# Performance work log

Hardware: AMD Instinct MI355X
Metric: run time of the kernel (lower is better)

Reference implementation:

```python
import jax, jax.numpy as jnp
import numpy as np

B, S, D = 8, 2048, 128

def setup_inputs() -> dict:
    key = jax.random.key(0)
    kq, kk, kv, km = jax.random.split(key, 4)
    q = jax.random.normal(kq, (B, S, D), dtype=jnp.float32)
    k = jax.random.normal(kk, (B, S, D), dtype=jnp.float32)
    v = jax.random.normal(kv, (B, S, D), dtype=jnp.float32)
    mask = jax.random.randint(km, (B, S), 0, 2).astype(bool)  # True = masked out
    return {"q": q, "k": k, "v": v, "mask": mask}

def reference(q, k, v, mask):
    scaler = np.sqrt(D).astype(np.float32)
    # score[b, i, j] = <q_i, k_j> / sqrt(d_k)
    score = jnp.einsum('bik,bjk->bij', q, k) / scaler
    score = score - jnp.max(score, axis=-1, keepdims=True)
    e = jnp.exp(score)
    # mask is (B, S_kv): broadcast across query positions, zero out masked keys
    e = jnp.where(mask[:, None, :], 0.0, e)
    a = e / jnp.sum(e, axis=-1, keepdims=True)
    c = jnp.einsum('bij,bjd->bid', a, v)
    return c
```

## Files before the change

kernel.cpp:

```cpp
#include <hip/hip_runtime.h>
#include <math.h>

typedef __attribute__((ext_vector_type(8))) short short8;
typedef __attribute__((ext_vector_type(4))) float floatx4;

namespace {
constexpr int Bn = 8;
constexpr int Sn = 2048;
constexpr int Dn = 128;
constexpr int BQ = 64;
constexpr int BK = 64;
constexpr int QTILES = Sn / BQ;
constexpr int NKB = Sn / BK;
constexpr int ROWS = Bn * Sn;
constexpr int NSPLIT = 4;
constexpr float SC2 = 0.12753102063642597f;
constexpr int TILE_USH = BK * Dn;
}

#if __has_builtin(__builtin_amdgcn_exp2f)
#define EXP2(x) __builtin_amdgcn_exp2f(x)
#else
#define EXP2(x) exp2f(x)
#endif

__device__ __forceinline__ unsigned short f2bf(float x) {
  union { float f; unsigned u; } a; a.f = x;
  unsigned r = a.u + 0x7fffu + ((a.u >> 16) & 1u);
  return (unsigned short)(r >> 16);
}

__device__ __forceinline__ void gl_lds16(const void* g, void* l, int lane) {
#if __has_builtin(__builtin_amdgcn_global_load_lds)
  (void)lane;
  __builtin_amdgcn_global_load_lds((const __attribute__((address_space(1))) unsigned int*)g,
                                   (__attribute__((address_space(3))) unsigned int*)l, 16, 0, 0);
#else
  *(float4*)((char*)l + lane * 16) = *(const float4*)g;
#endif
}

__global__ __launch_bounds__(256)
void prep(const float* __restrict__ kg, const float* __restrict__ vg,
          const unsigned char* __restrict__ mraw,
          unsigned short* __restrict__ Kpg, unsigned short* __restrict__ Vpg,
          float* __restrict__ mb2g) {
  __shared__ __align__(16) float Vf[64 * 136];
  const int p = blockIdx.x;
  const int b = p >> 5, kb = p & 31;
  const int t = threadIdx.x;

  unsigned wv = ((const unsigned int*)mraw)[t];
  int any1  = __syncthreads_or((wv & 0x0000ff00u) ? 1 : 0);
  int any23 = __syncthreads_or((wv & 0xffff0000u) ? 1 : 0);
  const int mlayout = any1 ? 1 : (any23 ? 2 : 0);
  if (kb == 0) {
    #pragma unroll
    for (int i = 0; i < 8; ++i) {
      int idx = i * 256 + t;
      int jj = b * Sn + idx;
      bool ms;
      if (mlayout == 1)      ms = mraw[jj] != 0;
      else if (mlayout == 2) ms = ((const float*)mraw)[jj] != 0.0f;
      else                   ms = ((const int*)mraw)[jj] != 0;
      mb2g[jj] = ms ? -1e30f : 0.0f;
    }
  }

  const int j  = t >> 2;
  const int og = t & 3;
  const size_t rowbase = ((size_t)(b * Sn + kb * 64 + j)) * 32 + og * 8;
  const float4* k4 = (const float4*)kg;
  const float4* v4 = (const float4*)vg;

  float4 kf[8];
  #pragma unroll
  for (int q = 0; q < 8; ++q) kf[q] = k4[rowbase + q];
  unsigned short* Krow = Kpg + (size_t)p * TILE_USH + j * 128;
  #pragma unroll
  for (int oo = 0; oo < 4; ++oo) {
    const int o = og * 4 + oo;
    short8 pk;
    float4 a = kf[oo * 2], bq = kf[oo * 2 + 1];
    pk[0] = (short)f2bf(a.x);  pk[1] = (short)f2bf(a.y);
    pk[2] = (short)f2bf(a.z);  pk[3] = (short)f2bf(a.w);
    pk[4] = (short)f2bf(bq.x); pk[5] = (short)f2bf(bq.y);
    pk[6] = (short)f2bf(bq.z); pk[7] = (short)f2bf(bq.w);
    *(short8*)(Krow + ((o ^ (j & 7)) * 8)) = pk;
  }

  #pragma unroll
  for (int q = 0; q < 8; ++q) {
    float4 f = v4[rowbase + q];
    *(float4*)&Vf[j * 136 + og * 32 + q * 4] = f;
  }
  __syncthreads();

  const int d = t >> 1, h = t & 1;
  unsigned short* Vrow = Vpg + (size_t)p * TILE_USH + d * 64;
  #pragma unroll
  for (int oo = 0; oo < 4; ++oo) {
    const int o = h * 4 + oo;
    short8 pk;
    #pragma unroll
    for (int i = 0; i < 8; ++i)
      pk[i] = (short)f2bf(Vf[(o * 8 + i) * 136 + d]);
    *(short8*)(Vrow + ((o ^ (d & 7)) * 8)) = pk;
  }
}

template<int SPLIT, bool DIRECT>
__global__ __launch_bounds__(256, 4)
void attn_fwd(const float* __restrict__ qg,
              const unsigned short* __restrict__ Kpg,
              const unsigned short* __restrict__ Vpg,
              const float* __restrict__ mb2g,
              float* __restrict__ outg, float* __restrict__ Op,
              float* __restrict__ Mp, float* __restrict__ Lp) {
  __shared__ __align__(16) unsigned short Khi[TILE_USH];
  __shared__ __align__(16) unsigned short Vt[TILE_USH];
  __shared__ __align__(16) unsigned short Pq[4 * 16 * 64];

  const int tid = threadIdx.x;
  const int bid = blockIdx.x;
  const int b   = bid & 7;
  const int q0  = ((bid >> 3) & (QTILES - 1)) * BQ;
  const int s   = bid >> 8;
  const int kb0 = s * (NKB / SPLIT);
  const int kbN = kb0 + NKB / SPLIT;
  const int w   = tid >> 6;
  const int L   = tid & 63;
  const int g   = L >> 4;
  const int c   = L & 15;
  const int sw  = c & 7;

  short8 qh[4], ql[4];
  {
    const float* qrow = qg + (size_t)(b * Sn + q0 + w * 16 + c) * Dn + g * 8;
    #pragma unroll
    for (int kk = 0; kk < 4; ++kk) {
      #pragma unroll
      for (int j = 0; j < 8; ++j) {
        float x = qrow[kk * 32 + j];
        unsigned short hi = f2bf(x);
        union { unsigned u; float f; } hv; hv.u = ((unsigned)hi) << 16;
        qh[kk][j] = (short)hi;
        ql[kk][j] = (short)f2bf(x - hv.f);
      }
    }
  }

  float m_i = -INFINITY, l_i = 0.0f;
  floatx4 O[8];
  #pragma unroll
  for (int n2 = 0; n2 < 8; ++n2) O[n2] = (floatx4){0.f, 0.f, 0.f, 0.f};

  unsigned short* pwave = Pq + w * 1024;
  const int stagebase = w * 4096;

  for (int kb = kb0; kb < kbN; ++kb) {
    __syncthreads();

    {
      const char* kt = (const char*)(Kpg + (size_t)(b * NKB + kb) * TILE_USH);
      const char* vt = (const char*)(Vpg + (size_t)(b * NKB + kb) * TILE_USH);
      #pragma unroll
      for (int i = 0; i < 4; ++i) {
        const int off = stagebase + i * 1024;
        gl_lds16(kt + off + L * 16, (char*)Khi + off, L);
        gl_lds16(vt + off + L * 16, (char*)Vt + off, L);
      }
    }
    __syncthreads();

    const float4* mb4 = (const float4*)(mb2g + b * Sn + kb * BK);
    float4 mbv[4];
    #pragma unroll
    for (int nt = 0; nt < 4; ++nt) mbv[nt] = mb4[nt * 4 + g];

    floatx4 acc[4];
    #pragma unroll
    for (int nt = 0; nt < 4; ++nt) acc[nt] = (floatx4){0.f, 0.f, 0.f, 0.f};
    #pragma unroll
    for (int kk = 0; kk < 4; ++kk) {
      const int ko = ((kk * 4 + g) ^ sw) * 8;
      #pragma unroll
      for (int nt = 0; nt < 4; ++nt) {
        short8 kf = *(const short8*)&Khi[(nt * 16 + c) * 128 + ko];
        acc[nt] = __builtin_amdgcn_mfma_f32_16x16x32_bf16(kf, qh[kk], acc[nt], 0, 0, 0);
        acc[nt] = __builtin_amdgcn_mfma_f32_16x16x32_bf16(kf, ql[kk], acc[nt], 0, 0, 0);
      }
    }

    #pragma unroll
    for (int nt = 0; nt < 4; ++nt) {
      acc[nt][0] = fmaf(acc[nt][0], SC2, mbv[nt].x);
      acc[nt][1] = fmaf(acc[nt][1], SC2, mbv[nt].y);
      acc[nt][2] = fmaf(acc[nt][2], SC2, mbv[nt].z);
      acc[nt][3] = fmaf(acc[nt][3], SC2, mbv[nt].w);
    }
    float mx = -INFINITY;
    #pragma unroll
    for (int nt = 0; nt < 4; ++nt)
      #pragma unroll
      for (int r = 0; r < 4; ++r) mx = fmaxf(mx, acc[nt][r]);
    mx = fmaxf(mx, __shfl_xor(mx, 16));
    mx = fmaxf(mx, __shfl_xor(mx, 32));
    const float mnew = fmaxf(m_i, mx);
    const float alpha = EXP2(m_i - mnew);
    float rs = 0.0f;
    #pragma unroll
    for (int nt = 0; nt < 4; ++nt)
      #pragma unroll
      for (int r = 0; r < 4; ++r) {
        float e = EXP2(acc[nt][r] - mnew);
        acc[nt][r] = e;
        rs += e;
      }
    rs += __shfl_xor(rs, 16);
    rs += __shfl_xor(rs, 32);
    l_i = l_i * alpha + rs;
    m_i = mnew;

    #pragma unroll
    for (int nt = 0; nt < 4; ++nt) {
      ushort4 pk = make_ushort4(f2bf(acc[nt][0]), f2bf(acc[nt][1]),
                                f2bf(acc[nt][2]), f2bf(acc[nt][3]));
      const int oct = nt * 2 + (g >> 1);
      *(ushort4*)&pwave[c * 64 + ((oct ^ sw) * 8) + (g & 1) * 4] = pk;
    }

    #pragma unroll
    for (int n2 = 0; n2 < 8; ++n2)
      #pragma unroll
      for (int r = 0; r < 4; ++r) O[n2][r] *= alpha;

    #pragma unroll
    for (int kk = 0; kk < 2; ++kk) {
      const int ko = ((kk * 4 + g) ^ sw) * 8;
      short8 pf = *(const short8*)&pwave[c * 64 + ko];
      #pragma unroll
      for (int n2 = 0; n2 < 8; ++n2) {
        short8 vf = *(const short8*)&Vt[(n2 * 16 + c) * 64 + ko];
        O[n2] = __builtin_amdgcn_mfma_f32_16x16x32_bf16(vf, pf, O[n2], 0, 0, 0);
      }
    }
  }

  const int rowbase = b * Sn + q0 + w * 16;
  if constexpr (DIRECT) {
    const float inv = 1.0f / l_i;
    float* orow = outg + (size_t)(rowbase + c) * Dn;
    #pragma unroll
    for (int n2 = 0; n2 < 8; ++n2) {
      float4 f = make_float4(O[n2][0] * inv, O[n2][1] * inv, O[n2][2] * inv, O[n2][3] * inv);
      *(float4*)&orow[n2 * 16 + g * 4] = f;
    }
  } else {
    float* orow = Op + ((size_t)s * ROWS + rowbase + c) * Dn;
    #pragma unroll
    for (int n2 = 0; n2 < 8; ++n2) {
      float4 f = make_float4(O[n2][0], O[n2][1], O[n2][2], O[n2][3]);
      *(float4*)&orow[n2 * 16 + g * 4] = f;
    }
    if (g == 0) {
      Mp[s * ROWS + rowbase + c] = m_i;
      Lp[s * ROWS + rowbase + c] = l_i;
    }
  }
}

__global__ __launch_bounds__(256)
void attn_combine(const float4* __restrict__ Op4, const float* __restrict__ Mp,
                  const float* __restrict__ Lp, float4* __restrict__ out4) {
  const int gid = blockIdx.x * 256 + threadIdx.x;
  const int row = gid >> 5;
  const int c4  = gid & 31;
  float ms[NSPLIT];
  float m = -INFINITY;
  #pragma unroll
  for (int s = 0; s < NSPLIT; ++s) { ms[s] = Mp[s * ROWS + row]; m = fmaxf(m, ms[s]); }
  float l = 0.0f;
  float4 acc = make_float4(0.f, 0.f, 0.f, 0.f);
  #pragma unroll
  for (int s = 0; s < NSPLIT; ++s) {
    float wgt = EXP2(ms[s] - m);
    l = fmaf(Lp[s * ROWS + row], wgt, l);
    float4 o = Op4[(size_t)(s * ROWS + row) * 32 + c4];
    acc.x = fmaf(o.x, wgt, acc.x);
    acc.y = fmaf(o.y, wgt, acc.y);
    acc.z = fmaf(o.z, wgt, acc.z);
    acc.w = fmaf(o.w, wgt, acc.w);
  }
  float inv = 1.0f / l;
  out4[(size_t)row * 32 + c4] = make_float4(acc.x * inv, acc.y * inv, acc.z * inv, acc.w * inv);
}

extern "C" void kernel_launch(void* const* d_in, const int* in_sizes, int n_in,
                              void* d_out, int out_size, void* d_ws, size_t ws_size,
                              hipStream_t stream) {
  const float* q = (const float*)d_in[0];
  const float* k = (const float*)d_in[1];
  const float* v = (const float*)d_in[2];
  const unsigned char* m = (const unsigned char*)d_in[3];
  float* out = (float*)d_out;
  (void)in_sizes; (void)n_in; (void)out_size;

  constexpr size_t OPB = (size_t)NSPLIT * ROWS * Dn * sizeof(float);
  constexpr size_t MLB = (size_t)NSPLIT * ROWS * sizeof(float);
  constexpr size_t KPB = (size_t)Bn * NKB * TILE_USH * 2;
  constexpr size_t MBB = (size_t)ROWS * sizeof(float);

  char* ws = (char*)d_ws;
  if (ws_size >= OPB + 2 * MLB + 2 * KPB + MBB) {
    float* Op = (float*)ws;
    float* Mp = (float*)(ws + OPB);
    float* Lp = (float*)(ws + OPB + MLB);
    unsigned short* Kp = (unsigned short*)(ws + OPB + 2 * MLB);
    unsigned short* Vp = (unsigned short*)(ws + OPB + 2 * MLB + KPB);
    float* mb2 = (float*)(ws + OPB + 2 * MLB + 2 * KPB);
    prep<<<dim3(Bn * NKB), dim3(256), 0, stream>>>(k, v, m, Kp, Vp, mb2);
    attn_fwd<NSPLIT, false><<<dim3(Bn * QTILES * NSPLIT), dim3(256), 0, stream>>>(
        q, Kp, Vp, mb2, out, Op, Mp, Lp);
    attn_combine<<<dim3(ROWS * 32 / 256), dim3(256), 0, stream>>>(
        (const float4*)Op, Mp, Lp, (float4*)out);
  } else if (ws_size >= 2 * KPB + MBB) {
    unsigned short* Kp = (unsigned short*)ws;
    unsigned short* Vp = (unsigned short*)(ws + KPB);
    float* mb2 = (float*)(ws + 2 * KPB);
    prep<<<dim3(Bn * NKB), dim3(256), 0, stream>>>(k, v, m, Kp, Vp, mb2);
    attn_fwd<1, true><<<dim3(Bn * QTILES), dim3(256), 0, stream>>>(
        q, Kp, Vp, mb2, out, nullptr, nullptr, nullptr);
  }
}
```

Baseline: 122.8 us.

## Use two-wave blocks with 32 query rows per wave, fp16 partials, finer prep grid

```diff
diff --git a/kernel.cpp b/kernel.cpp
--- a/kernel.cpp
+++ b/kernel.cpp
@@ -1,4 +1,5 @@
 #include <hip/hip_runtime.h>
+#include <hip/hip_fp16.h>
 #include <math.h>
 
 typedef __attribute__((ext_vector_type(8))) short short8;
@@ -45,81 +46,71 @@
           const unsigned char* __restrict__ mraw,
           unsigned short* __restrict__ Kpg, unsigned short* __restrict__ Vpg,
           float* __restrict__ mb2g) {
-  __shared__ __align__(16) float Vf[64 * 136];
+  __shared__ __align__(16) float Vf[16 * 136];
   const int p = blockIdx.x;
-  const int b = p >> 5, kb = p & 31;
+  const int b = p >> 7, q = p & 127;
+  const int kb = q >> 2, k16 = q & 3;
   const int t = threadIdx.x;
 
   unsigned wv = ((const unsigned int*)mraw)[t];
   int any1  = __syncthreads_or((wv & 0x0000ff00u) ? 1 : 0);
   int any23 = __syncthreads_or((wv & 0xffff0000u) ? 1 : 0);
   const int mlayout = any1 ? 1 : (any23 ? 2 : 0);
-  if (kb == 0) {
-    #pragma unroll
-    for (int i = 0; i < 8; ++i) {
-      int idx = i * 256 + t;
-      int jj = b * Sn + idx;
-      bool ms;
-      if (mlayout == 1)      ms = mraw[jj] != 0;
-      else if (mlayout == 2) ms = ((const float*)mraw)[jj] != 0.0f;
-      else                   ms = ((const int*)mraw)[jj] != 0;
-      mb2g[jj] = ms ? -1e30f : 0.0f;
-    }
-  }
-
-  const int j  = t >> 2;
-  const int og = t & 3;
-  const size_t rowbase = ((size_t)(b * Sn + kb * 64 + j)) * 32 + og * 8;
+  if (p < 64) {
+    int idx = p * 256 + t;
+    bool ms;
+    if (mlayout == 1)      ms = mraw[idx] != 0;
+    else if (mlayout == 2) ms = ((const float*)mraw)[idx] != 0.0f;
+    else                   ms = ((const int*)mraw)[idx] != 0;
+    mb2g[idx] = ms ? -1e30f : 0.0f;
+  }
+
+  const int j  = t >> 4;
+  const int o8 = t & 15;
+  const size_t base = ((size_t)(b * Sn + kb * 64 + k16 * 16 + j)) * 32 + o8 * 2;
   const float4* k4 = (const float4*)kg;
   const float4* v4 = (const float4*)vg;
 
-  float4 kf[8];
-  #pragma unroll
-  for (int q = 0; q < 8; ++q) kf[q] = k4[rowbase + q];
-  unsigned short* Krow = Kpg + (size_t)p * TILE_USH + j * 128;
-  #pragma unroll
-  for (int oo = 0; oo < 4; ++oo) {
-    const int o = og * 4 + oo;
+  {
+    float4 a = k4[base], bq = k4[base + 1];
     short8 pk;
-    float4 a = kf[oo * 2], bq = kf[oo * 2 + 1];
     pk[0] = (short)f2bf(a.x);  pk[1] = (short)f2bf(a.y);
     pk[2] = (short)f2bf(a.z);  pk[3] = (short)f2bf(a.w);
     pk[4] = (short)f2bf(bq.x); pk[5] = (short)f2bf(bq.y);
     pk[6] = (short)f2bf(bq.z); pk[7] = (short)f2bf(bq.w);
-    *(short8*)(Krow + ((o ^ (j & 7)) * 8)) = pk;
-  }
-
-  #pragma unroll
-  for (int q = 0; q < 8; ++q) {
-    float4 f = v4[rowbase + q];
-    *(float4*)&Vf[j * 136 + og * 32 + q * 4] = f;
+    const int jl = k16 * 16 + j;
+    *(short8*)(Kpg + (size_t)(b * NKB + kb) * TILE_USH + jl * 128 + ((o8 ^ (jl & 7)) * 8)) = pk;
+  }
+
+  {
+    float4 a = v4[base], bq = v4[base + 1];
+    *(float4*)&Vf[j * 136 + o8 * 8]     = a;
+    *(float4*)&Vf[j * 136 + o8 * 8 + 4] = bq;
   }
   __syncthreads();
 
-  const int d = t >> 1, h = t & 1;
-  unsigned short* Vrow = Vpg + (size_t)p * TILE_USH + d * 64;
-  #pragma unroll
-  for (int oo = 0; oo < 4; ++oo) {
-    const int o = h * 4 + oo;
-    short8 pk;
+  {
+    const int d = t >> 1, h = t & 1;
+    short8 pv;
     #pragma unroll
     for (int i = 0; i < 8; ++i)
-      pk[i] = (short)f2bf(Vf[(o * 8 + i) * 136 + d]);
-    *(short8*)(Vrow + ((o ^ (d & 7)) * 8)) = pk;
+      pv[i] = (short)f2bf(Vf[(h * 8 + i) * 136 + d]);
+    const int og = k16 * 2 + h;
+    *(short8*)(Vpg + (size_t)(b * NKB + kb) * TILE_USH + d * 64 + ((og ^ (d & 7)) * 8)) = pv;
   }
 }
 
 template<int SPLIT, bool DIRECT>
-__global__ __launch_bounds__(256, 4)
+__global__ __launch_bounds__(128, 2)
 void attn_fwd(const float* __restrict__ qg,
               const unsigned short* __restrict__ Kpg,
               const unsigned short* __restrict__ Vpg,
               const float* __restrict__ mb2g,
-              float* __restrict__ outg, float* __restrict__ Op,
+              float* __restrict__ outg, __half* __restrict__ Op,
               float* __restrict__ Mp, float* __restrict__ Lp) {
   __shared__ __align__(16) unsigned short Khi[TILE_USH];
   __shared__ __align__(16) unsigned short Vt[TILE_USH];
-  __shared__ __align__(16) unsigned short Pq[4 * 16 * 64];
+  __shared__ __align__(16) unsigned short Pq[2 * 2048];
 
   const int tid = threadIdx.x;
   const int bid = blockIdx.x;
@@ -134,9 +125,10 @@
   const int c   = L & 15;
   const int sw  = c & 7;
 
-  short8 qh[4], ql[4];
-  {
-    const float* qrow = qg + (size_t)(b * Sn + q0 + w * 16 + c) * Dn + g * 8;
+  short8 qh[2][4], ql[2][4];
+  #pragma unroll
+  for (int s2 = 0; s2 < 2; ++s2) {
+    const float* qrow = qg + (size_t)(b * Sn + q0 + w * 32 + s2 * 16 + c) * Dn + g * 8;
     #pragma unroll
     for (int kk = 0; kk < 4; ++kk) {
       #pragma unroll
@@ -144,28 +136,29 @@
         float x = qrow[kk * 32 + j];
         unsigned short hi = f2bf(x);
         union { unsigned u; float f; } hv; hv.u = ((unsigned)hi) << 16;
-        qh[kk][j] = (short)hi;
-        ql[kk][j] = (short)f2bf(x - hv.f);
-      }
-    }
-  }
-
-  float m_i = -INFINITY, l_i = 0.0f;
-  floatx4 O[8];
-  #pragma unroll
-  for (int n2 = 0; n2 < 8; ++n2) O[n2] = (floatx4){0.f, 0.f, 0.f, 0.f};
-
-  unsigned short* pwave = Pq + w * 1024;
-  const int stagebase = w * 4096;
+        qh[s2][kk][j] = (short)hi;
+        ql[s2][kk][j] = (short)f2bf(x - hv.f);
+      }
+    }
+  }
+
+  float m_i[2] = {-INFINITY, -INFINITY}, l_i[2] = {0.0f, 0.0f};
+  floatx4 O[2][8];
+  #pragma unroll
+  for (int s2 = 0; s2 < 2; ++s2)
+    #pragma unroll
+    for (int n2 = 0; n2 < 8; ++n2) O[s2][n2] = (floatx4){0.f, 0.f, 0.f, 0.f};
+
+  unsigned short* pwave = Pq + w * 2048;
+  const int stagebase = w * 8192;
 
   for (int kb = kb0; kb < kbN; ++kb) {
     __syncthreads();
-
     {
       const char* kt = (const char*)(Kpg + (size_t)(b * NKB + kb) * TILE_USH);
       const char* vt = (const char*)(Vpg + (size_t)(b * NKB + kb) * TILE_USH);
       #pragma unroll
-      for (int i = 0; i < 4; ++i) {
+      for (int i = 0; i < 8; ++i) {
         const int off = stagebase + i * 1024;
         gl_lds16(kt + off + L * 16, (char*)Khi + off, L);
         gl_lds16(vt + off + L * 16, (char*)Vt + off, L);
@@ -178,100 +171,120 @@
     #pragma unroll
     for (int nt = 0; nt < 4; ++nt) mbv[nt] = mb4[nt * 4 + g];
 
-    floatx4 acc[4];
-    #pragma unroll
-    for (int nt = 0; nt < 4; ++nt) acc[nt] = (floatx4){0.f, 0.f, 0.f, 0.f};
+    floatx4 acc[2][4];
+    #pragma unroll
+    for (int s2 = 0; s2 < 2; ++s2)
+      #pragma unroll
+      for (int nt = 0; nt < 4; ++nt) acc[s2][nt] = (floatx4){0.f, 0.f, 0.f, 0.f};
     #pragma unroll
     for (int kk = 0; kk < 4; ++kk) {
       const int ko = ((kk * 4 + g) ^ sw) * 8;
       #pragma unroll
       for (int nt = 0; nt < 4; ++nt) {
         short8 kf = *(const short8*)&Khi[(nt * 16 + c) * 128 + ko];
-        acc[nt] = __builtin_amdgcn_mfma_f32_16x16x32_bf16(kf, qh[kk], acc[nt], 0, 0, 0);
-        acc[nt] = __builtin_amdgcn_mfma_f32_16x16x32_bf16(kf, ql[kk], acc[nt], 0, 0, 0);
-      }
-    }
-
-    #pragma unroll
-    for (int nt = 0; nt < 4; ++nt) {
-      acc[nt][0] = fmaf(acc[nt][0], SC2, mbv[nt].x);
-      acc[nt][1] = fmaf(acc[nt][1], SC2, mbv[nt].y);
-      acc[nt][2] = fmaf(acc[nt][2], SC2, mbv[nt].z);
-      acc[nt][3] = fmaf(acc[nt][3], SC2, mbv[nt].w);
-    }
-    float mx = -INFINITY;
-    #pragma unroll
-    for (int nt = 0; nt < 4; ++nt)
-      #pragma unroll
-      for (int r = 0; r < 4; ++r) mx = fmaxf(mx, acc[nt][r]);
-    mx = fmaxf(mx, __shfl_xor(mx, 16));
-    mx = fmaxf(mx, __shfl_xor(mx, 32));
-    const float mnew = fmaxf(m_i, mx);
-    const float alpha = EXP2(m_i - mnew);
-    float rs = 0.0f;
-    #pragma unroll
-    for (int nt = 0; nt < 4; ++nt)
-      #pragma unroll
-      for (int r = 0; r < 4; ++r) {
-        float e = EXP2(acc[nt][r] - mnew);
-        acc[nt][r] = e;
-        rs += e;
-      }
-    rs += __shfl_xor(rs, 16);
-    rs += __shfl_xor(rs, 32);
-    l_i = l_i * alpha + rs;
-    m_i = mnew;
-
-    #pragma unroll
-    for (int nt = 0; nt < 4; ++nt) {
-      ushort4 pk = make_ushort4(f2bf(acc[nt][0]), f2bf(acc[nt][1]),
-                                f2bf(acc[nt][2]), f2bf(acc[nt][3]));
-      const int oct = nt * 2 + (g >> 1);
-      *(ushort4*)&pwave[c * 64 + ((oct ^ sw) * 8) + (g & 1) * 4] = pk;
-    }
-
-    #pragma unroll
-    for (int n2 = 0; n2 < 8; ++n2)
-      #pragma unroll
-      for (int r = 0; r < 4; ++r) O[n2][r] *= alpha;
+        acc[0][nt] = __builtin_amdgcn_mfma_f32_16x16x32_bf16(kf, qh[0][kk], acc[0][nt], 0, 0, 0);
+        acc[0][nt] = __builtin_amdgcn_mfma_f32_16x16x32_bf16(kf, ql[0][kk], acc[0][nt], 0, 0, 0);
+        acc[1][nt] = __builtin_amdgcn_mfma_f32_16x16x32_bf16(kf, qh[1][kk], acc[1][nt], 0, 0, 0);
+        acc[1][nt] = __builtin_amdgcn_mfma_f32_16x16x32_bf16(kf, ql[1][kk], acc[1][nt], 0, 0, 0);
+      }
+    }
+
+    float alpha[2];
+    #pragma unroll
+    for (int s2 = 0; s2 < 2; ++s2) {
+      #pragma unroll
+      for (int nt = 0; nt < 4; ++nt) {
+        acc[s2][nt][0] = fmaf(acc[s2][nt][0], SC2, mbv[nt].x);
+        acc[s2][nt][1] = fmaf(acc[s2][nt][1], SC2, mbv[nt].y);
+        acc[s2][nt][2] = fmaf(acc[s2][nt][2], SC2, mbv[nt].z);
+        acc[s2][nt][3] = fmaf(acc[s2][nt][3], SC2, mbv[nt].w);
+      }
+      float mx = -INFINITY;
+      #pragma unroll
+      for (int nt = 0; nt < 4; ++nt)
+        #pragma unroll
+        for (int r = 0; r < 4; ++r) mx = fmaxf(mx, acc[s2][nt][r]);
+      mx = fmaxf(mx, __shfl_xor(mx, 16));
+      mx = fmaxf(mx, __shfl_xor(mx, 32));
+      const float mnew = fmaxf(m_i[s2], mx);
+      alpha[s2] = EXP2(m_i[s2] - mnew);
+      float rs = 0.0f;
+      #pragma unroll
+      for (int nt = 0; nt < 4; ++nt)
+        #pragma unroll
+        for (int r = 0; r < 4; ++r) {
+          float e = EXP2(acc[s2][nt][r] - mnew);
+          acc[s2][nt][r] = e;
+          rs += e;
+        }
+      rs += __shfl_xor(rs, 16);
+      rs += __shfl_xor(rs, 32);
+      l_i[s2] = l_i[s2] * alpha[s2] + rs;
+      m_i[s2] = mnew;
+    }
+
+    #pragma unroll
+    for (int s2 = 0; s2 < 2; ++s2)
+      #pragma unroll
+      for (int nt = 0; nt < 4; ++nt) {
+        ushort4 pk = make_ushort4(f2bf(acc[s2][nt][0]), f2bf(acc[s2][nt][1]),
+                                  f2bf(acc[s2][nt][2]), f2bf(acc[s2][nt][3]));
+        const int oct = nt * 2 + (g >> 1);
+        *(ushort4*)&pwave[s2 * 1024 + c * 64 + ((oct ^ sw) * 8) + (g & 1) * 4] = pk;
+      }
+
+    #pragma unroll
+    for (int s2 = 0; s2 < 2; ++s2)
+      #pragma unroll
+      for (int n2 = 0; n2 < 8; ++n2)
+        #pragma unroll
+        for (int r = 0; r < 4; ++r) O[s2][n2][r] *= alpha[s2];
 
     #pragma unroll
     for (int kk = 0; kk < 2; ++kk) {
       const int ko = ((kk * 4 + g) ^ sw) * 8;
-      short8 pf = *(const short8*)&pwave[c * 64 + ko];
+      short8 pf0 = *(const short8*)&pwave[c * 64 + ko];
+      short8 pf1 = *(const short8*)&pwave[1024 + c * 64 + ko];
       #pragma unroll
       for (int n2 = 0; n2 < 8; ++n2) {
         short8 vf = *(const short8*)&Vt[(n2 * 16 + c) * 64 + ko];
-        O[n2] = __builtin_amdgcn_mfma_f32_16x16x32_bf16(vf, pf, O[n2], 0, 0, 0);
-      }
-    }
-  }
-
-  const int rowbase = b * Sn + q0 + w * 16;
-  if constexpr (DIRECT) {
-    const float inv = 1.0f / l_i;
-    float* orow = outg + (size_t)(rowbase + c) * Dn;
-    #pragma unroll
-    for (int n2 = 0; n2 < 8; ++n2) {
-      float4 f = make_float4(O[n2][0] * inv, O[n2][1] * inv, O[n2][2] * inv, O[n2][3] * inv);
-      *(float4*)&orow[n2 * 16 + g * 4] = f;
-    }
-  } else {
-    float* orow = Op + ((size_t)s * ROWS + rowbase + c) * Dn;
-    #pragma unroll
-    for (int n2 = 0; n2 < 8; ++n2) {
-      float4 f = make_float4(O[n2][0], O[n2][1], O[n2][2], O[n2][3]);
-      *(float4*)&orow[n2 * 16 + g * 4] = f;
-    }
-    if (g == 0) {
-      Mp[s * ROWS + rowbase + c] = m_i;
-      Lp[s * ROWS + rowbase + c] = l_i;
+        O[0][n2] = __builtin_amdgcn_mfma_f32_16x16x32_bf16(vf, pf0, O[0][n2], 0, 0, 0);
+        O[1][n2] = __builtin_amdgcn_mfma_f32_16x16x32_bf16(vf, pf1, O[1][n2], 0, 0, 0);
+      }
+    }
+  }
+
+  #pragma unroll
+  for (int s2 = 0; s2 < 2; ++s2) {
+    const int rowbase = b * Sn + q0 + w * 32 + s2 * 16 + c;
+    if constexpr (DIRECT) {
+      const float inv = 1.0f / l_i[s2];
+      float* orow = outg + (size_t)rowbase * Dn;
+      #pragma unroll
+      for (int n2 = 0; n2 < 8; ++n2) {
+        float4 f = make_float4(O[s2][n2][0] * inv, O[s2][n2][1] * inv,
+                               O[s2][n2][2] * inv, O[s2][n2][3] * inv);
+        *(float4*)&orow[n2 * 16 + g * 4] = f;
+      }
+    } else {
+      __half* orow = Op + ((size_t)s * ROWS + rowbase) * Dn;
+      #pragma unroll
+      for (int n2 = 0; n2 < 8; ++n2) {
+        union { __half2 h2[2]; uint2 u; } pk;
+        pk.h2[0] = __floats2half2_rn(O[s2][n2][0], O[s2][n2][1]);
+        pk.h2[1] = __floats2half2_rn(O[s2][n2][2], O[s2][n2][3]);
+        *(uint2*)&orow[n2 * 16 + g * 4] = pk.u;
+      }
+      if (g == 0) {
+        Mp[s * ROWS + rowbase] = m_i[s2];
+        Lp[s * ROWS + rowbase] = l_i[s2];
+      }
     }
   }
 }
 
 __global__ __launch_bounds__(256)
-void attn_combine(const float4* __restrict__ Op4, const float* __restrict__ Mp,
+void attn_combine(const __half* __restrict__ Op, const float* __restrict__ Mp,
                   const float* __restrict__ Lp, float4* __restrict__ out4) {
   const int gid = blockIdx.x * 256 + threadIdx.x;
   const int row = gid >> 5;
@@ -286,11 +299,14 @@
   for (int s = 0; s < NSPLIT; ++s) {
     float wgt = EXP2(ms[s] - m);
     l = fmaf(Lp[s * ROWS + row], wgt, l);
-    float4 o = Op4[(size_t)(s * ROWS + row) * 32 + c4];
-    acc.x = fmaf(o.x, wgt, acc.x);
-    acc.y = fmaf(o.y, wgt, acc.y);
-    acc.z = fmaf(o.z, wgt, acc.z);
-    acc.w = fmaf(o.w, wgt, acc.w);
+    union { uint2 u; __half2 h2[2]; } pk;
+    pk.u = ((const uint2*)Op)[(size_t)(s * ROWS + row) * 32 + c4];
+    float2 f0 = __half22float2(pk.h2[0]);
+    float2 f1 = __half22float2(pk.h2[1]);
+    acc.x = fmaf(f0.x, wgt, acc.x);
+    acc.y = fmaf(f0.y, wgt, acc.y);
+    acc.z = fmaf(f1.x, wgt, acc.z);
+    acc.w = fmaf(f1.y, wgt, acc.w);
   }
   float inv = 1.0f / l;
   out4[(size_t)row * 32 + c4] = make_float4(acc.x * inv, acc.y * inv, acc.z * inv, acc.w * inv);
@@ -306,30 +322,30 @@
   float* out = (float*)d_out;
   (void)in_sizes; (void)n_in; (void)out_size;
 
-  constexpr size_t OPB = (size_t)NSPLIT * ROWS * Dn * sizeof(float);
+  constexpr size_t OPB = (size_t)NSPLIT * ROWS * Dn * sizeof(__half);
   constexpr size_t MLB = (size_t)NSPLIT * ROWS * sizeof(float);
   constexpr size_t KPB = (size_t)Bn * NKB * TILE_USH * 2;
   constexpr size_t MBB = (size_t)ROWS * sizeof(float);
 
   char* ws = (char*)d_ws;
   if (ws_size >= OPB + 2 * MLB + 2 * KPB + MBB) {
-    float* Op = (float*)ws;
+    __half* Op = (__half*)ws;
     float* Mp = (float*)(ws + OPB);
     float* Lp = (float*)(ws + OPB + MLB);
     unsigned short* Kp = (unsigned short*)(ws + OPB + 2 * MLB);
     unsigned short* Vp = (unsigned short*)(ws + OPB + 2 * MLB + KPB);
     float* mb2 = (float*)(ws + OPB + 2 * MLB + 2 * KPB);
-    prep<<<dim3(Bn * NKB), dim3(256), 0, stream>>>(k, v, m, Kp, Vp, mb2);
-    attn_fwd<NSPLIT, false><<<dim3(Bn * QTILES * NSPLIT), dim3(256), 0, stream>>>(
+    prep<<<dim3(Bn * NKB * 4), dim3(256), 0, stream>>>(k, v, m, Kp, Vp, mb2);
+    attn_fwd<NSPLIT, false><<<dim3(Bn * QTILES * NSPLIT), dim3(128), 0, stream>>>(
         q, Kp, Vp, mb2, out, Op, Mp, Lp);
     attn_combine<<<dim3(ROWS * 32 / 256), dim3(256), 0, stream>>>(
-        (const float4*)Op, Mp, Lp, (float4*)out);
+        Op, Mp, Lp, (float4*)out);
   } else if (ws_size >= 2 * KPB + MBB) {
     unsigned short* Kp = (unsigned short*)ws;
     unsigned short* Vp = (unsigned short*)(ws + KPB);
     float* mb2 = (float*)(ws + 2 * KPB);
-    prep<<<dim3(Bn * NKB), dim3(256), 0, stream>>>(k, v, m, Kp, Vp, mb2);
-    attn_fwd<1, true><<<dim3(Bn * QTILES), dim3(256), 0, stream>>>(
+    prep<<<dim3(Bn * NKB * 4), dim3(256), 0, stream>>>(k, v, m, Kp, Vp, mb2);
+    attn_fwd<1, true><<<dim3(Bn * QTILES), dim3(128), 0, stream>>>(
         q, Kp, Vp, mb2, out, nullptr, nullptr, nullptr);
   }
 }
```

New measurement: 120.1 us. -2.2%, faster.
